# Optimization experiments

Measured on AMD Instinct MI355X. Metric: run time of the kernel, lower is better.

Reference implementation:

```python
import jax, jax.numpy as jnp
import numpy as np

NEG = -1e9  # additive mask value for padded keys


def layer_norm(x, g, b, eps=1e-5):
    m = x.mean(-1, keepdims=True)
    v = ((x - m) ** 2).mean(-1, keepdims=True)
    return (x - m) / jnp.sqrt(v + eps) * g + b


def setup_inputs() -> dict:
    key = jax.random.key(0)
    G, n, H, heads, L, F, De, deg = 64, 256, 256, 8, 4, 512, 16, 32
    N = G * n
    E = N * deg
    ks = jax.random.split(key, 24)
    s = 0.02
    node_embs = jax.random.normal(ks[0], (N, H), jnp.float32)
    batch_vec = jnp.arange(N, dtype=jnp.int32) // n          # [N] sorted graph ids
    ptr = jnp.arange(G + 1, dtype=jnp.int32) * n              # [G+1]
    epg = E // G
    g_idx = jnp.repeat(jnp.arange(G, dtype=jnp.int32), epg)
    src = g_idx * n + jax.random.randint(ks[1], (E,), 0, n)
    dst = g_idx * n + jax.random.randint(ks[2], (E,), 0, n)
    edge_index = jnp.stack([src, dst])                        # [2,E] intra-graph edges
    edge_attr = jax.random.normal(ks[3], (E, De), jnp.float32)
    return {
        "node_embs": node_embs, "batch_vec": batch_vec, "ptr": ptr,
        "edge_index": edge_index, "edge_attr": edge_attr,
        "edge_proj_w": jax.random.normal(ks[4], (heads, De), jnp.float32) * s,
        "edge_proj_b": jnp.zeros((heads,), jnp.float32),
        "Wqkv": jax.random.normal(ks[5], (L, 3 * H, H), jnp.float32) * s,
        "bqkv": jnp.zeros((L, 3 * H), jnp.float32),
        "Wo": jax.random.normal(ks[6], (L, H, H), jnp.float32) * s,
        "bo": jnp.zeros((L, H), jnp.float32),
        "ln1_g": jnp.ones((L, H), jnp.float32), "ln1_b": jnp.zeros((L, H), jnp.float32),
        "ln2_g": jnp.ones((L, H), jnp.float32), "ln2_b": jnp.zeros((L, H), jnp.float32),
        "W1": jax.random.normal(ks[7], (L, F, H), jnp.float32) * s,
        "b1": jnp.zeros((L, F), jnp.float32),
        "W2": jax.random.normal(ks[8], (L, H, F), jnp.float32) * s,
        "b2": jnp.zeros((L, H), jnp.float32),
        "norm_g": jnp.ones((H,), jnp.float32), "norm_b": jnp.zeros((H,), jnp.float32),
    }


def reference(node_embs, batch_vec, ptr, edge_index, edge_attr,
              edge_proj_w, edge_proj_b, Wqkv, bqkv, Wo, bo,
              ln1_g, ln1_b, ln2_g, ln2_b, W1, b1, W2, b2, norm_g, norm_b):
    N, H = node_embs.shape
    G = ptr.shape[0] - 1
    maxN = N // G  # graphs are equal-sized -> static max_N
    L = Wqkv.shape[0]
    heads = edge_proj_w.shape[0]
    dh = H // heads

    # to_dense_batch: scatter nodes into [G, maxN, H] with validity mask
    local = jnp.arange(N) - ptr[batch_vec]
    dense = jnp.zeros((G, maxN, H), node_embs.dtype).at[batch_vec, local].set(node_embs)
    valid = jnp.zeros((G, maxN), bool).at[batch_vec, local].set(True)

    # scatter-add per-head edge bias -> [G, heads, maxN, maxN]
    src, dst = edge_index[0], edge_index[1]
    g = batch_vec[src]
    sl = src - ptr[g]
    dl = dst - ptr[g]
    ea = edge_attr @ edge_proj_w.T + edge_proj_b  # [E, heads]
    bias = jnp.zeros((G, maxN, maxN, heads), ea.dtype).at[g, sl, dl].add(ea)
    bias = bias.transpose(0, 3, 1, 2)

    pad = jnp.where(valid, 0.0, NEG)[:, None, None, :]  # [G,1,1,maxN] key padding
    mask = bias + pad
    scale = 1.0 / np.sqrt(dh)

    x = dense
    for i in range(L):  # pre-norm TransformerEncoderLayer (relu activation)
        y = layer_norm(x, ln1_g[i], ln1_b[i])
        qkv = y @ Wqkv[i].T + bqkv[i]
        q, k, v = jnp.split(qkv, 3, -1)
        q = q.reshape(G, maxN, heads, dh).transpose(0, 2, 1, 3)
        k = k.reshape(G, maxN, heads, dh).transpose(0, 2, 1, 3)
        v = v.reshape(G, maxN, heads, dh).transpose(0, 2, 1, 3)
        scores = jnp.einsum('ghqd,ghkd->ghqk', q, k) * scale + mask
        p = jax.nn.softmax(scores, axis=-1)
        o = jnp.einsum('ghqk,ghkd->ghqd', p, v).transpose(0, 2, 1, 3).reshape(G, maxN, H)
        x = x + o @ Wo[i].T + bo[i]
        y2 = layer_norm(x, ln2_g[i], ln2_b[i])
        x = x + jax.nn.relu(y2 @ W1[i].T + b1[i]) @ W2[i].T + b2[i]

    out = layer_norm(x, norm_g, norm_b)
    return (out * valid[..., None]).sum(axis=1)  # [G, H] sum-pool over valid nodes
```

## Files before the change

kernel.cpp:

```cpp
#include <hip/hip_runtime.h>
#include <hip/hip_bf16.h>

#define GG   64
#define NPG  256
#define NN   16384
#define HH   256
#define HEADS 8
#define DH   32
#define LAYERS 4
#define FF   512
#define DE   16
#define NE   524288
#define EPG  8192
#define ECAP 224

typedef __attribute__((ext_vector_type(8))) short bf16x8_t;
typedef __attribute__((ext_vector_type(4))) short s16x4;
typedef __attribute__((ext_vector_type(4))) float f32x4;
typedef __attribute__((ext_vector_type(4))) unsigned int u32x4;

typedef const __attribute__((address_space(1))) char gchar_t;
typedef __attribute__((address_space(3))) char lchar_t;

__device__ __forceinline__ float b2f(short u) {
    return __uint_as_float(((unsigned int)(unsigned short)u) << 16);
}
__device__ __forceinline__ short f2b(float f) {
    __hip_bfloat16 h = __float2bfloat16(f);
    return *reinterpret_cast<short*>(&h);
}
__device__ __forceinline__ unsigned pack2(float a, float b) {
    return ((unsigned)(unsigned short)f2b(a)) | (((unsigned)(unsigned short)f2b(b)) << 16);
}

__global__ __launch_bounds__(256) void f2b_kernel(const float* __restrict__ in,
                                                  __hip_bfloat16* __restrict__ out,
                                                  int nelem) {
    int i = blockIdx.x * 256 + threadIdx.x;
    if (i < nelem) out[i] = __float2bfloat16(in[i]);
}

__global__ void sentinel_kernel(float* out, float v, int n) {
    int i = blockIdx.x * 256 + threadIdx.x;
    if (i < n) out[i] = v;
}

__global__ __launch_bounds__(256) void edge_bucket_kernel(const int* __restrict__ eidx,
                                                          int* __restrict__ cnt,
                                                          int* __restrict__ eb) {
    int e = blockIdx.x * 256 + threadIdx.x;
    int s = eidx[e];
    int bucket = ((s >> 8) << 6) | ((s & 255) >> 2);
    int slot = atomicAdd(&cnt[bucket], 1);
    if (slot < ECAP) eb[bucket * ECAP + slot] = e;
}

__global__ __launch_bounds__(256) void edge_bias_fused(const int* __restrict__ eidx,
                                                       const float* __restrict__ eattr,
                                                       const float* __restrict__ pw,
                                                       const float* __restrict__ pb,
                                                       const int* __restrict__ cnt,
                                                       const int* __restrict__ eb,
                                                       __hip_bfloat16* __restrict__ out) {
    __shared__ float acc[4][NPG][HEADS];
    __shared__ float pwl[HEADS][DE];
    __shared__ float pbl[HEADS];
    int tid = threadIdx.x;
    int bid = blockIdx.x;
    int g = bid >> 6, blk = bid & 63;

    f32x4* az = (f32x4*)acc;
#pragma unroll
    for (int i = 0; i < 8; ++i) az[i * 256 + tid] = f32x4{0, 0, 0, 0};
    if (tid < HEADS * DE) ((float*)pwl)[tid] = pw[tid];
    if (tid < HEADS) pbl[tid] = pb[tid];
    __syncthreads();

    int n = cnt[bid];
    if (n > ECAP) n = ECAP;
    const int* lst = eb + bid * ECAP;
    for (int base = tid; base < n * 8; base += 256) {
        int e = lst[base >> 3];
        int h = base & 7;
        int s = eidx[e];
        int d = eidx[NE + e];
        int slL = s & 3;
        int dl = d & 255;
        const f32x4* ap = (const f32x4*)(eattr + (size_t)e * DE);
        f32x4 a0 = ap[0], a1 = ap[1], a2 = ap[2], a3 = ap[3];
        const float* w = pwl[h];
        float v = pbl[h];
        v += a0[0]*w[0] + a0[1]*w[1] + a0[2]*w[2] + a0[3]*w[3];
        v += a1[0]*w[4] + a1[1]*w[5] + a1[2]*w[6] + a1[3]*w[7];
        v += a2[0]*w[8] + a2[1]*w[9] + a2[2]*w[10] + a2[3]*w[11];
        v += a3[0]*w[12] + a3[1]*w[13] + a3[2]*w[14] + a3[3]*w[15];
        atomicAdd(&acc[slL][dl][h], v);
    }
    __syncthreads();

    __hip_bfloat16* base = out + (size_t)g * HEADS * NPG * NPG + (size_t)blk * 4 * NPG;
#pragma unroll
    for (int h = 0; h < HEADS; ++h)
#pragma unroll
        for (int slL = 0; slL < 4; ++slL)
            base[(size_t)h * NPG * NPG + slL * NPG + tid] = __float2bfloat16(acc[slL][tid][h]);
}

__global__ __launch_bounds__(256) void ln_kernel(const float* __restrict__ x,
                                                 const float* __restrict__ gam,
                                                 const float* __restrict__ bet,
                                                 __hip_bfloat16* __restrict__ y) {
    int wave = threadIdx.x >> 6, lane = threadIdx.x & 63;
    int row = blockIdx.x * 4 + wave;
    f32x4 v = ((const f32x4*)x)[(size_t)row * 64 + lane];
    float s1 = v[0] + v[1] + v[2] + v[3];
    float s2 = v[0]*v[0] + v[1]*v[1] + v[2]*v[2] + v[3]*v[3];
#pragma unroll
    for (int off = 32; off > 0; off >>= 1) {
        s1 += __shfl_xor(s1, off, 64);
        s2 += __shfl_xor(s2, off, 64);
    }
    float mean = s1 * (1.f / HH);
    float var  = s2 * (1.f / HH) - mean * mean;
    float rs = rsqrtf(var + 1e-5f);
    f32x4 gm = ((const f32x4*)gam)[lane];
    f32x4 bt = ((const f32x4*)bet)[lane];
    s16x4 o;
#pragma unroll
    for (int k = 0; k < 4; ++k) o[k] = f2b((v[k] - mean) * rs * gm[k] + bt[k]);
    *(s16x4*)(((short*)y) + (size_t)row * HH + lane * 4) = o;
}

template <int K, int EPI>
__global__ __launch_bounds__(256) void gemm_kernel(const __hip_bfloat16* __restrict__ A,
                                                   const __hip_bfloat16* __restrict__ W,
                                                   const float* __restrict__ bias,
                                                   void* __restrict__ outv, int O) {
    __shared__ __hip_bfloat16 Al[128 * 64];
    __shared__ __hip_bfloat16 Wl[128 * 64];
    int tile_m = blockIdx.x * 128, tile_n = blockIdx.y * 128;
    int tid = threadIdx.x;
    int lane = tid & 63, wave = tid >> 6;
    int wm = wave >> 1, wn = wave & 1;
    int l15 = lane & 15, kq = (lane >> 4) * 8;
    f32x4 acc[4][4] = {};
    for (int p = 0; p < K / 64; ++p) {
        __syncthreads();
#pragma unroll
        for (int j = 0; j < 4; ++j) {
            int c = j * 256 + tid;
            int row = c >> 3, kc = c & 7;
            int kcs = kc ^ (row & 7);
            const char* ga = (const char*)(A + (size_t)(tile_m + row) * K + p * 64) + kcs * 16;
            const char* gw = (const char*)(W + (size_t)(tile_n + row) * K + p * 64) + kcs * 16;
            __builtin_amdgcn_global_load_lds((gchar_t*)ga, (lchar_t*)((char*)Al + c * 16), 16, 0, 0);
            __builtin_amdgcn_global_load_lds((gchar_t*)gw, (lchar_t*)((char*)Wl + c * 16), 16, 0, 0);
        }
        __syncthreads();
#pragma unroll
        for (int k0 = 0; k0 < 64; k0 += 32) {
            int k2 = (k0 + kq) * 2;
            bf16x8_t a[4], b[4];
#pragma unroll
            for (int i = 0; i < 4; ++i) {
                int ra = wm * 64 + i * 16 + l15;
                a[i] = *(const bf16x8_t*)((const char*)Al + ra * 128 + (k2 ^ ((ra & 7) << 4)));
                int rb = wn * 64 + i * 16 + l15;
                b[i] = *(const bf16x8_t*)((const char*)Wl + rb * 128 + (k2 ^ ((rb & 7) << 4)));
            }
#pragma unroll
            for (int i = 0; i < 4; ++i)
#pragma unroll
                for (int jj = 0; jj < 4; ++jj)
                    acc[i][jj] = __builtin_amdgcn_mfma_f32_16x16x32_bf16(a[i], b[jj], acc[i][jj], 0, 0, 0);
        }
    }
    int rbase = tile_m + wm * 64 + ((lane >> 4) << 2);
#pragma unroll
    for (int i = 0; i < 4; ++i) {
#pragma unroll
        for (int jj = 0; jj < 4; ++jj) {
            int col = tile_n + wn * 64 + jj * 16 + l15;
            float bc = bias[col];
#pragma unroll
            for (int r = 0; r < 4; ++r) {
                size_t idx = (size_t)(rbase + i * 16 + r) * O + col;
                float v = acc[i][jj][r] + bc;
                if (EPI == 1) ((float*)outv)[idx] += v;
                else if (EPI == 2) ((__hip_bfloat16*)outv)[idx] = __float2bfloat16(fmaxf(v, 0.f));
                else ((__hip_bfloat16*)outv)[idx] = __float2bfloat16(v);
            }
        }
    }
}

__global__ __launch_bounds__(256) void attn_mfma(const __hip_bfloat16* __restrict__ QKV,
                                                 const __hip_bfloat16* __restrict__ BIAS,
                                                 __hip_bfloat16* __restrict__ OB) {
    __shared__ short Kl[256 * 40];
    __shared__ short VTl[32 * 264];
    int g = blockIdx.x >> 3, h = blockIdx.x & 7;
    int tid = threadIdx.x;
    int lane = tid & 63, w = tid >> 6;
    int l15 = lane & 15, lg = lane >> 4;
    const __hip_bfloat16* qb = QKV + (size_t)g * NPG * 768 + h * DH;

#pragma unroll
    for (int it = 0; it < 4; ++it) {
        int c = it * 256 + tid;
        int r = c >> 2, seg = c & 3;
        bf16x8_t kv8 = *(const bf16x8_t*)(qb + (size_t)r * 768 + HH + seg * 8);
        *(bf16x8_t*)(&Kl[r * 40 + seg * 8]) = kv8;
        bf16x8_t vv8 = *(const bf16x8_t*)(qb + (size_t)r * 768 + 2 * HH + seg * 8);
#pragma unroll
        for (int j = 0; j < 8; ++j) VTl[(seg * 8 + j) * 264 + r] = vv8[j];
    }

    bf16x8_t qf[4];
#pragma unroll
    for (int qt = 0; qt < 4; ++qt)
        qf[qt] = *(const bf16x8_t*)(qb + (size_t)(64 * w + 16 * qt + l15) * 768 + lg * 8);

    const short* bp = (const short*)BIAS + ((size_t)(g * 8 + h) << 16);
    const float SCALE = 0.17677669529663687f;

    f32x4 oacc[2][4] = {};
    float ls[4] = {0.f, 0.f, 0.f, 0.f};
    __syncthreads();

    for (int kc = 0; kc < 8; ++kc) {
        int kbase = kc * 32;
        bf16x8_t ka0 = *(const bf16x8_t*)(&Kl[(kbase + l15) * 40 + lg * 8]);
        bf16x8_t ka1 = *(const bf16x8_t*)(&Kl[(kbase + 16 + l15) * 40 + lg * 8]);
        s16x4 bl[2][4];
#pragma unroll
        for (int f = 0; f < 2; ++f)
#pragma unroll
            for (int qt = 0; qt < 4; ++qt) {
                int q = 64 * w + 16 * qt + l15;
                bl[f][qt] = *(const s16x4*)(bp + (size_t)q * 256 + kbase + 16 * f + 4 * lg);
            }
        f32x4 st[2][4];
        f32x4 zz = {0.f, 0.f, 0.f, 0.f};
#pragma unroll
        for (int qt = 0; qt < 4; ++qt) {
            st[0][qt] = __builtin_amdgcn_mfma_f32_16x16x32_bf16(ka0, qf[qt], zz, 0, 0, 0);
            st[1][qt] = __builtin_amdgcn_mfma_f32_16x16x32_bf16(ka1, qf[qt], zz, 0, 0, 0);
        }
        unsigned pk[2][4][2];
#pragma unroll
        for (int f = 0; f < 2; ++f)
#pragma unroll
            for (int qt = 0; qt < 4; ++qt) {
                float p0 = __expf(fmaf(st[f][qt][0], SCALE, b2f(bl[f][qt][0]) - 8.f));
                float p1 = __expf(fmaf(st[f][qt][1], SCALE, b2f(bl[f][qt][1]) - 8.f));
                float p2 = __expf(fmaf(st[f][qt][2], SCALE, b2f(bl[f][qt][2]) - 8.f));
                float p3 = __expf(fmaf(st[f][qt][3], SCALE, b2f(bl[f][qt][3]) - 8.f));
                ls[qt] += (p0 + p1) + (p2 + p3);
                pk[f][qt][0] = pack2(p0, p1);
                pk[f][qt][1] = pack2(p2, p3);
            }
        bf16x8_t bq[4];
#pragma unroll
        for (int qt = 0; qt < 4; ++qt) {
            u32x4 wv;
#pragma unroll
            for (int wi = 0; wi < 4; ++wi) {
                int pr = wi & 1;
                int src = ((2 * lg + (wi >> 1)) & 3) * 16 + l15;
                unsigned t0 = (unsigned)__shfl((int)pk[0][qt][pr], src, 64);
                unsigned t1 = (unsigned)__shfl((int)pk[1][qt][pr], src, 64);
                wv[wi] = (lg < 2) ? t0 : t1;
            }
            bq[qt] = __builtin_bit_cast(bf16x8_t, wv);
        }
        bf16x8_t va0 = *(const bf16x8_t*)(&VTl[l15 * 264 + kbase + lg * 8]);
        bf16x8_t va1 = *(const bf16x8_t*)(&VTl[(16 + l15) * 264 + kbase + lg * 8]);
#pragma unroll
        for (int qt = 0; qt < 4; ++qt) {
            oacc[0][qt] = __builtin_amdgcn_mfma_f32_16x16x32_bf16(va0, bq[qt], oacc[0][qt], 0, 0, 0);
            oacc[1][qt] = __builtin_amdgcn_mfma_f32_16x16x32_bf16(va1, bq[qt], oacc[1][qt], 0, 0, 0);
        }
    }
    float inv[4];
#pragma unroll
    for (int qt = 0; qt < 4; ++qt) {
        float t = ls[qt];
        t += __shfl_xor(t, 16, 64);
        t += __shfl_xor(t, 32, 64);
        inv[qt] = 1.f / t;
    }
#pragma unroll
    for (int dt = 0; dt < 2; ++dt)
#pragma unroll
        for (int qt = 0; qt < 4; ++qt) {
            size_t q = (size_t)g * NPG + 64 * w + 16 * qt + l15;
#pragma unroll
            for (int pr = 0; pr < 2; ++pr) {
                unsigned pkd = pack2(oacc[dt][qt][2 * pr] * inv[qt],
                                     oacc[dt][qt][2 * pr + 1] * inv[qt]);
                *(unsigned*)((short*)OB + q * HH + h * 32 + 16 * dt + 4 * lg + 2 * pr) = pkd;
            }
        }
}

__global__ __launch_bounds__(256) void pool_kernel(const float* __restrict__ x,
                                                   const float* __restrict__ gam,
                                                   const float* __restrict__ bet,
                                                   float* __restrict__ out) {
    int g = blockIdx.x >> 3;
    int chunk = (blockIdx.x & 7) * 32;
    int wave = threadIdx.x >> 6, lane = threadIdx.x & 63;
    f32x4 gm = ((const f32x4*)gam)[lane];
    f32x4 bt = ((const f32x4*)bet)[lane];
    float a0 = 0, a1 = 0, a2 = 0, a3 = 0;
#pragma unroll
    for (int it = 0; it < 8; ++it) {
        int row = g * NPG + chunk + it * 4 + wave;
        f32x4 v = ((const f32x4*)x)[(size_t)row * 64 + lane];
        float s1 = v[0] + v[1] + v[2] + v[3];
        float s2 = v[0]*v[0] + v[1]*v[1] + v[2]*v[2] + v[3]*v[3];
#pragma unroll
        for (int off = 32; off > 0; off >>= 1) {
            s1 += __shfl_xor(s1, off, 64);
            s2 += __shfl_xor(s2, off, 64);
        }
        float mean = s1 * (1.f / HH);
        float var  = s2 * (1.f / HH) - mean * mean;
        float rs = rsqrtf(var + 1e-5f);
        a0 += (v[0] - mean) * rs * gm[0] + bt[0];
        a1 += (v[1] - mean) * rs * gm[1] + bt[1];
        a2 += (v[2] - mean) * rs * gm[2] + bt[2];
        a3 += (v[3] - mean) * rs * gm[3] + bt[3];
    }
    float* ob = out + g * HH + lane * 4;
    atomicAdd(ob + 0, a0);
    atomicAdd(ob + 1, a1);
    atomicAdd(ob + 2, a2);
    atomicAdd(ob + 3, a3);
}

extern "C" void kernel_launch(void* const* d_in, const int* in_sizes, int n_in,
                              void* d_out, int out_size, void* d_ws, size_t ws_size,
                              hipStream_t stream) {
    const float* node_embs = (const float*)d_in[0];
    const int*   eidx      = (const int*)d_in[3];
    const float* eattr     = (const float*)d_in[4];
    const float* pw        = (const float*)d_in[5];
    const float* pb        = (const float*)d_in[6];
    const float* Wqkv      = (const float*)d_in[7];
    const float* bqkv      = (const float*)d_in[8];
    const float* Wo        = (const float*)d_in[9];
    const float* bo        = (const float*)d_in[10];
    const float* ln1_g     = (const float*)d_in[11];
    const float* ln1_b     = (const float*)d_in[12];
    const float* ln2_g     = (const float*)d_in[13];
    const float* ln2_b     = (const float*)d_in[14];
    const float* W1        = (const float*)d_in[15];
    const float* b1        = (const float*)d_in[16];
    const float* W2        = (const float*)d_in[17];
    const float* b2        = (const float*)d_in[18];
    const float* norm_g    = (const float*)d_in[19];
    const float* norm_b    = (const float*)d_in[20];

    const size_t SZ_BIASB = (size_t)GG * HEADS * NPG * NPG * 2;
    const size_t SZ_X     = (size_t)NN * HH * 4;
    const size_t SZ_QKV   = (size_t)NN * 768 * 2;
    const size_t SZ_YB    = (size_t)NN * HH * 2;
    const size_t SZ_OB    = SZ_YB;
    const size_t SZ_H1    = (size_t)NN * FF * 2;
    const size_t SZ_CNT   = (size_t)GG * 64 * 4;
    const size_t SZ_EB    = (size_t)GG * 64 * ECAP * 4;
    const size_t SZ_WQKV  = (size_t)LAYERS * 768 * HH * 2;
    const size_t SZ_WO    = (size_t)LAYERS * HH * HH * 2;
    const size_t SZ_W1    = (size_t)LAYERS * FF * HH * 2;
    const size_t SZ_W2    = (size_t)LAYERS * HH * FF * 2;
    const size_t NEEDED = SZ_BIASB + SZ_X + SZ_QKV + SZ_YB + SZ_OB + SZ_H1 +
                          SZ_CNT + SZ_EB + SZ_WQKV + SZ_WO + SZ_W1 + SZ_W2;
    if (ws_size < NEEDED) {
        sentinel_kernel<<<(out_size + 255) / 256, 256, 0, stream>>>(
            (float*)d_out, (float)(ws_size >> 20), out_size);
        return;
    }

    char* w = (char*)d_ws;
    __hip_bfloat16* BIASB = (__hip_bfloat16*)w; w += SZ_BIASB;
    float* X = (float*)w;                       w += SZ_X;
    __hip_bfloat16* QKVB = (__hip_bfloat16*)w;  w += SZ_QKV;
    __hip_bfloat16* YB   = (__hip_bfloat16*)w;  w += SZ_YB;
    __hip_bfloat16* OB   = (__hip_bfloat16*)w;  w += SZ_OB;
    __hip_bfloat16* H1   = (__hip_bfloat16*)w;  w += SZ_H1;
    int* CNT = (int*)w;                         w += SZ_CNT;
    int* EB  = (int*)w;                         w += SZ_EB;
    __hip_bfloat16* WqkvB = (__hip_bfloat16*)w; w += SZ_WQKV;
    __hip_bfloat16* WoB   = (__hip_bfloat16*)w; w += SZ_WO;
    __hip_bfloat16* W1B   = (__hip_bfloat16*)w; w += SZ_W1;
    __hip_bfloat16* W2B   = (__hip_bfloat16*)w; w += SZ_W2;

    hipMemsetAsync(d_out, 0, (size_t)out_size * 4, stream);
    hipMemsetAsync(CNT, 0, SZ_CNT, stream);
    hipMemcpyAsync(X, node_embs, SZ_X, hipMemcpyDeviceToDevice, stream);

    f2b_kernel<<<LAYERS * 768 * HH / 256, 256, 0, stream>>>(Wqkv, WqkvB, LAYERS * 768 * HH);
    f2b_kernel<<<LAYERS * HH * HH / 256, 256, 0, stream>>>(Wo, WoB, LAYERS * HH * HH);
    f2b_kernel<<<LAYERS * FF * HH / 256, 256, 0, stream>>>(W1, W1B, LAYERS * FF * HH);
    f2b_kernel<<<LAYERS * HH * FF / 256, 256, 0, stream>>>(W2, W2B, LAYERS * HH * FF);

    edge_bucket_kernel<<<NE / 256, 256, 0, stream>>>(eidx, CNT, EB);
    edge_bias_fused<<<GG * 64, 256, 0, stream>>>(eidx, eattr, pw, pb, CNT, EB, BIASB);

    for (int i = 0; i < LAYERS; i++) {
        ln_kernel<<<NN / 4, 256, 0, stream>>>(X, ln1_g + i * HH, ln1_b + i * HH, YB);
        gemm_kernel<256, 3><<<dim3(NN / 128, 768 / 128), 256, 0, stream>>>(
            YB, WqkvB + (size_t)i * 768 * HH, bqkv + i * 768, QKVB, 768);
        attn_mfma<<<GG * HEADS, 256, 0, stream>>>(QKVB, BIASB, OB);
        gemm_kernel<256, 1><<<dim3(NN / 128, HH / 128), 256, 0, stream>>>(
            OB, WoB + (size_t)i * HH * HH, bo + i * HH, X, HH);
        ln_kernel<<<NN / 4, 256, 0, stream>>>(X, ln2_g + i * HH, ln2_b + i * HH, YB);
        gemm_kernel<256, 2><<<dim3(NN / 128, FF / 128), 256, 0, stream>>>(
            YB, W1B + (size_t)i * FF * HH, b1 + i * FF, H1, FF);
        gemm_kernel<512, 1><<<dim3(NN / 128, HH / 128), 256, 0, stream>>>(
            H1, W2B + (size_t)i * HH * FF, b2 + i * HH, X, HH);
    }

    pool_kernel<<<GG * 8, 256, 0, stream>>>(X, norm_g, norm_b, (float*)d_out);
}
```

Before: 673.5 us.

## Double-buffer smaller GEMM tiles and precompute edge bias projection per edge

The GEMM kernel moves from 128x128 to 64x64 output tiles with double-buffered LDS staging, so the next K-slice loads while the current one computes, and the grid has four times as many blocks. Edge attributes are projected to per-head bf16 values once per edge in a new kernel instead of inside the scatter kernel. The edge buckets are halved to two source rows each, with the edge list staged in LDS. Smaller tiles reduce per-block data reuse and raise global traffic, and the lower ECAP of 160 risks dropping edges if a bucket overflows.

```diff
diff --git a/kernel.cpp b/kernel.cpp
--- a/kernel.cpp
+++ b/kernel.cpp
@@ -12,7 +12,7 @@
 #define DE   16
 #define NE   524288
 #define EPG  8192
-#define ECAP 224
+#define ECAP 160
 
 typedef __attribute__((ext_vector_type(8))) short bf16x8_t;
 typedef __attribute__((ext_vector_type(4))) short s16x4;
@@ -45,65 +45,79 @@
     if (i < n) out[i] = v;
 }
 
-__global__ __launch_bounds__(256) void edge_bucket_kernel(const int* __restrict__ eidx,
-                                                          int* __restrict__ cnt,
-                                                          int* __restrict__ eb) {
-    int e = blockIdx.x * 256 + threadIdx.x;
-    int s = eidx[e];
-    int bucket = ((s >> 8) << 6) | ((s & 255) >> 2);
-    int slot = atomicAdd(&cnt[bucket], 1);
-    if (slot < ECAP) eb[bucket * ECAP + slot] = e;
-}
-
-__global__ __launch_bounds__(256) void edge_bias_fused(const int* __restrict__ eidx,
-                                                       const float* __restrict__ eattr,
-                                                       const float* __restrict__ pw,
-                                                       const float* __restrict__ pb,
-                                                       const int* __restrict__ cnt,
-                                                       const int* __restrict__ eb,
-                                                       __hip_bfloat16* __restrict__ out) {
-    __shared__ float acc[4][NPG][HEADS];
+__global__ __launch_bounds__(256) void ea_kernel(const float* __restrict__ eattr,
+                                                 const float* __restrict__ pw,
+                                                 const float* __restrict__ pb,
+                                                 __hip_bfloat16* __restrict__ ea) {
     __shared__ float pwl[HEADS][DE];
     __shared__ float pbl[HEADS];
-    int tid = threadIdx.x;
-    int bid = blockIdx.x;
-    int g = bid >> 6, blk = bid & 63;
-
-    f32x4* az = (f32x4*)acc;
-#pragma unroll
-    for (int i = 0; i < 8; ++i) az[i * 256 + tid] = f32x4{0, 0, 0, 0};
-    if (tid < HEADS * DE) ((float*)pwl)[tid] = pw[tid];
-    if (tid < HEADS) pbl[tid] = pb[tid];
+    if (threadIdx.x < HEADS * DE) ((float*)pwl)[threadIdx.x] = pw[threadIdx.x];
+    if (threadIdx.x < HEADS) pbl[threadIdx.x] = pb[threadIdx.x];
     __syncthreads();
-
-    int n = cnt[bid];
-    if (n > ECAP) n = ECAP;
-    const int* lst = eb + bid * ECAP;
-    for (int base = tid; base < n * 8; base += 256) {
-        int e = lst[base >> 3];
-        int h = base & 7;
-        int s = eidx[e];
-        int d = eidx[NE + e];
-        int slL = s & 3;
-        int dl = d & 255;
-        const f32x4* ap = (const f32x4*)(eattr + (size_t)e * DE);
-        f32x4 a0 = ap[0], a1 = ap[1], a2 = ap[2], a3 = ap[3];
+    int e = blockIdx.x * 256 + threadIdx.x;
+    const f32x4* ap = (const f32x4*)(eattr + (size_t)e * DE);
+    f32x4 a0 = ap[0], a1 = ap[1], a2 = ap[2], a3 = ap[3];
+    bf16x8_t o;
+#pragma unroll
+    for (int h = 0; h < HEADS; ++h) {
         const float* w = pwl[h];
         float v = pbl[h];
         v += a0[0]*w[0] + a0[1]*w[1] + a0[2]*w[2] + a0[3]*w[3];
         v += a1[0]*w[4] + a1[1]*w[5] + a1[2]*w[6] + a1[3]*w[7];
         v += a2[0]*w[8] + a2[1]*w[9] + a2[2]*w[10] + a2[3]*w[11];
         v += a3[0]*w[12] + a3[1]*w[13] + a3[2]*w[14] + a3[3]*w[15];
+        o[h] = f2b(v);
+    }
+    *(bf16x8_t*)((short*)ea + (size_t)e * 8) = o;
+}
+
+__global__ __launch_bounds__(256) void edge_bucket_kernel(const int* __restrict__ eidx,
+                                                          int* __restrict__ cnt,
+                                                          int* __restrict__ eb) {
+    int e = blockIdx.x * 256 + threadIdx.x;
+    int s = eidx[e];
+    int bucket = ((s >> 8) << 7) | ((s & 255) >> 1);
+    int slot = atomicAdd(&cnt[bucket], 1);
+    if (slot < ECAP) eb[bucket * ECAP + slot] = e;
+}
+
+__global__ __launch_bounds__(256) void edge_bias_fused(const int* __restrict__ eidx,
+                                                       const __hip_bfloat16* __restrict__ ea,
+                                                       const int* __restrict__ cnt,
+                                                       const int* __restrict__ eb,
+                                                       __hip_bfloat16* __restrict__ out) {
+    __shared__ float acc[2][NPG][HEADS];
+    __shared__ int lst[ECAP];
+    int tid = threadIdx.x;
+    int bid = blockIdx.x;
+    int g = bid >> 7, blk = bid & 127;
+
+    f32x4* az = (f32x4*)acc;
+#pragma unroll
+    for (int i = 0; i < 4; ++i) az[i * 256 + tid] = f32x4{0, 0, 0, 0};
+    int n = cnt[bid];
+    if (n > ECAP) n = ECAP;
+    for (int i = tid; i < n; i += 256) lst[i] = eb[bid * ECAP + i];
+    __syncthreads();
+
+    for (int base = tid; base < n * 8; base += 256) {
+        int e = lst[base >> 3];
+        int h = base & 7;
+        int s = eidx[e];
+        int d = eidx[NE + e];
+        int slL = s & 1;
+        int dl = d & 255;
+        float v = b2f((short)((const unsigned short*)ea)[(size_t)e * 8 + h]);
         atomicAdd(&acc[slL][dl][h], v);
     }
     __syncthreads();
 
-    __hip_bfloat16* base = out + (size_t)g * HEADS * NPG * NPG + (size_t)blk * 4 * NPG;
+    __hip_bfloat16* basep = out + (size_t)g * HEADS * NPG * NPG + (size_t)blk * 2 * NPG;
 #pragma unroll
     for (int h = 0; h < HEADS; ++h)
 #pragma unroll
-        for (int slL = 0; slL < 4; ++slL)
-            base[(size_t)h * NPG * NPG + slL * NPG + tid] = __float2bfloat16(acc[slL][tid][h]);
+        for (int slL = 0; slL < 2; ++slL)
+            basep[(size_t)h * NPG * NPG + slL * NPG + tid] = __float2bfloat16(acc[slL][tid][h]);
 }
 
 __global__ __launch_bounds__(256) void ln_kernel(const float* __restrict__ x,
@@ -136,51 +150,61 @@
                                                    const __hip_bfloat16* __restrict__ W,
                                                    const float* __restrict__ bias,
                                                    void* __restrict__ outv, int O) {
-    __shared__ __hip_bfloat16 Al[128 * 64];
-    __shared__ __hip_bfloat16 Wl[128 * 64];
-    int tile_m = blockIdx.x * 128, tile_n = blockIdx.y * 128;
+    __shared__ __hip_bfloat16 Al[2][64 * 64];
+    __shared__ __hip_bfloat16 Wl[2][64 * 64];
+    int tile_m = blockIdx.x * 64, tile_n = blockIdx.y * 64;
     int tid = threadIdx.x;
     int lane = tid & 63, wave = tid >> 6;
     int wm = wave >> 1, wn = wave & 1;
     int l15 = lane & 15, kq = (lane >> 4) * 8;
-    f32x4 acc[4][4] = {};
-    for (int p = 0; p < K / 64; ++p) {
-        __syncthreads();
-#pragma unroll
-        for (int j = 0; j < 4; ++j) {
+    constexpr int NT = K / 64;
+    f32x4 acc[2][2] = {};
+
+    auto STAGE = [&](int buf, int p) {
+#pragma unroll
+        for (int j = 0; j < 2; ++j) {
             int c = j * 256 + tid;
             int row = c >> 3, kc = c & 7;
             int kcs = kc ^ (row & 7);
             const char* ga = (const char*)(A + (size_t)(tile_m + row) * K + p * 64) + kcs * 16;
             const char* gw = (const char*)(W + (size_t)(tile_n + row) * K + p * 64) + kcs * 16;
-            __builtin_amdgcn_global_load_lds((gchar_t*)ga, (lchar_t*)((char*)Al + c * 16), 16, 0, 0);
-            __builtin_amdgcn_global_load_lds((gchar_t*)gw, (lchar_t*)((char*)Wl + c * 16), 16, 0, 0);
-        }
-        __syncthreads();
+            __builtin_amdgcn_global_load_lds((gchar_t*)ga, (lchar_t*)((char*)&Al[buf][0] + c * 16), 16, 0, 0);
+            __builtin_amdgcn_global_load_lds((gchar_t*)gw, (lchar_t*)((char*)&Wl[buf][0] + c * 16), 16, 0, 0);
+        }
+    };
+
+    STAGE(0, 0);
+    __syncthreads();
+    int cur = 0;
+    for (int t = 0; t < NT; ++t) {
+        if (t + 1 < NT) STAGE(cur ^ 1, t + 1);
 #pragma unroll
         for (int k0 = 0; k0 < 64; k0 += 32) {
             int k2 = (k0 + kq) * 2;
-            bf16x8_t a[4], b[4];
-#pragma unroll
-            for (int i = 0; i < 4; ++i) {
-                int ra = wm * 64 + i * 16 + l15;
-                a[i] = *(const bf16x8_t*)((const char*)Al + ra * 128 + (k2 ^ ((ra & 7) << 4)));
-                int rb = wn * 64 + i * 16 + l15;
-                b[i] = *(const bf16x8_t*)((const char*)Wl + rb * 128 + (k2 ^ ((rb & 7) << 4)));
-            }
-#pragma unroll
-            for (int i = 0; i < 4; ++i)
-#pragma unroll
-                for (int jj = 0; jj < 4; ++jj)
+            bf16x8_t a[2], b[2];
+#pragma unroll
+            for (int i = 0; i < 2; ++i) {
+                int ra = wm * 32 + i * 16 + l15;
+                a[i] = *(const bf16x8_t*)((const char*)&Al[cur][0] + ra * 128 + (k2 ^ ((ra & 7) << 4)));
+                int rb = wn * 32 + i * 16 + l15;
+                b[i] = *(const bf16x8_t*)((const char*)&Wl[cur][0] + rb * 128 + (k2 ^ ((rb & 7) << 4)));
+            }
+#pragma unroll
+            for (int i = 0; i < 2; ++i)
+#pragma unroll
+                for (int jj = 0; jj < 2; ++jj)
                     acc[i][jj] = __builtin_amdgcn_mfma_f32_16x16x32_bf16(a[i], b[jj], acc[i][jj], 0, 0, 0);
         }
-    }
-    int rbase = tile_m + wm * 64 + ((lane >> 4) << 2);
-#pragma unroll
-    for (int i = 0; i < 4; ++i) {
-#pragma unroll
-        for (int jj = 0; jj < 4; ++jj) {
-            int col = tile_n + wn * 64 + jj * 16 + l15;
+        __syncthreads();
+        cur ^= 1;
+    }
+
+    int rbase = tile_m + wm * 32 + ((lane >> 4) << 2);
+#pragma unroll
+    for (int i = 0; i < 2; ++i) {
+#pragma unroll
+        for (int jj = 0; jj < 2; ++jj) {
+            int col = tile_n + wn * 32 + jj * 16 + l15;
             float bc = bias[col];
 #pragma unroll
             for (int r = 0; r < 4; ++r) {
@@ -369,14 +393,15 @@
     const size_t SZ_YB    = (size_t)NN * HH * 2;
     const size_t SZ_OB    = SZ_YB;
     const size_t SZ_H1    = (size_t)NN * FF * 2;
-    const size_t SZ_CNT   = (size_t)GG * 64 * 4;
-    const size_t SZ_EB    = (size_t)GG * 64 * ECAP * 4;
+    const size_t SZ_EA    = (size_t)NE * HEADS * 2;
+    const size_t SZ_CNT   = (size_t)GG * 128 * 4;
+    const size_t SZ_EB    = (size_t)GG * 128 * ECAP * 4;
     const size_t SZ_WQKV  = (size_t)LAYERS * 768 * HH * 2;
     const size_t SZ_WO    = (size_t)LAYERS * HH * HH * 2;
     const size_t SZ_W1    = (size_t)LAYERS * FF * HH * 2;
     const size_t SZ_W2    = (size_t)LAYERS * HH * FF * 2;
     const size_t NEEDED = SZ_BIASB + SZ_X + SZ_QKV + SZ_YB + SZ_OB + SZ_H1 +
-                          SZ_CNT + SZ_EB + SZ_WQKV + SZ_WO + SZ_W1 + SZ_W2;
+                          SZ_EA + SZ_CNT + SZ_EB + SZ_WQKV + SZ_WO + SZ_W1 + SZ_W2;
     if (ws_size < NEEDED) {
         sentinel_kernel<<<(out_size + 255) / 256, 256, 0, stream>>>(
             (float*)d_out, (float)(ws_size >> 20), out_size);
@@ -390,6 +415,7 @@
     __hip_bfloat16* YB   = (__hip_bfloat16*)w;  w += SZ_YB;
     __hip_bfloat16* OB   = (__hip_bfloat16*)w;  w += SZ_OB;
     __hip_bfloat16* H1   = (__hip_bfloat16*)w;  w += SZ_H1;
+    __hip_bfloat16* EA   = (__hip_bfloat16*)w;  w += SZ_EA;
     int* CNT = (int*)w;                         w += SZ_CNT;
     int* EB  = (int*)w;                         w += SZ_EB;
     __hip_bfloat16* WqkvB = (__hip_bfloat16*)w; w += SZ_WQKV;
@@ -406,20 +432,21 @@
     f2b_kernel<<<LAYERS * FF * HH / 256, 256, 0, stream>>>(W1, W1B, LAYERS * FF * HH);
     f2b_kernel<<<LAYERS * HH * FF / 256, 256, 0, stream>>>(W2, W2B, LAYERS * HH * FF);
 
+    ea_kernel<<<NE / 256, 256, 0, stream>>>(eattr, pw, pb, EA);
     edge_bucket_kernel<<<NE / 256, 256, 0, stream>>>(eidx, CNT, EB);
-    edge_bias_fused<<<GG * 64, 256, 0, stream>>>(eidx, eattr, pw, pb, CNT, EB, BIASB);
+    edge_bias_fused<<<GG * 128, 256, 0, stream>>>(eidx, EA, CNT, EB, BIASB);
 
     for (int i = 0; i < LAYERS; i++) {
         ln_kernel<<<NN / 4, 256, 0, stream>>>(X, ln1_g + i * HH, ln1_b + i * HH, YB);
-        gemm_kernel<256, 3><<<dim3(NN / 128, 768 / 128), 256, 0, stream>>>(
+        gemm_kernel<256, 3><<<dim3(NN / 64, 768 / 64), 256, 0, stream>>>(
             YB, WqkvB + (size_t)i * 768 * HH, bqkv + i * 768, QKVB, 768);
         attn_mfma<<<GG * HEADS, 256, 0, stream>>>(QKVB, BIASB, OB);
-        gemm_kernel<256, 1><<<dim3(NN / 128, HH / 128), 256, 0, stream>>>(
+        gemm_kernel<256, 1><<<dim3(NN / 64, HH / 64), 256, 0, stream>>>(
             OB, WoB + (size_t)i * HH * HH, bo + i * HH, X, HH);
         ln_kernel<<<NN / 4, 256, 0, stream>>>(X, ln2_g + i * HH, ln2_b + i * HH, YB);
-        gemm_kernel<256, 2><<<dim3(NN / 128, FF / 128), 256, 0, stream>>>(
+        gemm_kernel<256, 2><<<dim3(NN / 64, FF / 64), 256, 0, stream>>>(
             YB, W1B + (size_t)i * FF * HH, b1 + i * FF, H1, FF);
-        gemm_kernel<512, 1><<<dim3(NN / 128, HH / 128), 256, 0, stream>>>(
+        gemm_kernel<512, 1><<<dim3(NN / 64, HH / 64), 256, 0, stream>>>(
             H1, W2B + (size_t)i * HH * FF, b2 + i * HH, X, HH);
     }
 
```

Measured after the change: 623.7 us. 7.4% less time.
